# Optimization experiments

Measured on AMD Instinct MI355X. Metric: run time of the kernel, lower is better.

## Reference

```python
import jax, jax.numpy as jnp
import numpy as np

B = 2048
IN_FEATURES = 512
OUT_FEATURES = 32768
S = 64.0   # arcface default scale
M = 0.5    # arcface default margin
EPS = 1e-7


def _l2_normalize(x, axis=-1):
    # matches torch F.normalize(p=2, eps=1e-12)
    n = jnp.sqrt(jnp.sum(x * x, axis=axis, keepdims=True))
    return x / jnp.maximum(n, 1e-12)


def setup_inputs() -> dict:
    key = jax.random.key(0)
    k1, k2, k3 = jax.random.split(key, 3)
    features = jax.random.normal(k1, (B, IN_FEATURES), dtype=jnp.float32)
    y_true = jax.random.randint(k2, (B,), 0, OUT_FEATURES)
    # xavier_uniform_ for weight of shape (out, in)
    limit = float(np.sqrt(6.0 / (OUT_FEATURES + IN_FEATURES)))
    weight = jax.random.uniform(k3, (OUT_FEATURES, IN_FEATURES), dtype=jnp.float32,
                                minval=-limit, maxval=limit)
    return {"features": features, "y_true": y_true, "weight": weight}


def reference(features, y_true, weight):
    f = _l2_normalize(features)            # [B, D]
    w = _l2_normalize(weight)              # [C, D]
    wf = jnp.einsum('bd,cd->bc', f, w)     # [B, C] cosine logits
    tgt = wf[jnp.arange(wf.shape[0]), y_true]  # [B]
    # arcface margin transform
    numerator = S * jnp.cos(jnp.arccos(jnp.clip(tgt, -1.0 + EPS, 1.0 - EPS)) + M)
    # sum of exp(s*wf) over all non-target classes = full sum minus target term
    excl_sum = jnp.sum(jnp.exp(S * wf), axis=1) - jnp.exp(S * tgt)
    denominator = jnp.exp(numerator) + excl_sum
    L = numerator - jnp.log(denominator)
    return -jnp.mean(L)
```

## Files before the change

kernel.cpp:

```cpp
#include <hip/hip_runtime.h>
#include <hip/hip_bf16.h>
#include <math.h>


#define BN 2048
#define DK 512
#define CN 32768

typedef __attribute__((ext_vector_type(4))) float floatx4;
typedef __attribute__((ext_vector_type(2))) long longx2;

__device__ inline float dot4(floatx4 a, floatx4 b) {
  return a.x * b.x + a.y * b.y + a.z * b.z + a.w * b.w;
}

__device__ inline int pack_fp8x4(floatx4 v) {
  int r = __builtin_amdgcn_cvt_pk_fp8_f32(v.x, v.y, 0, false);
  r = __builtin_amdgcn_cvt_pk_fp8_f32(v.z, v.w, r, true);
  return r;
}

__device__ inline int permute16(int j) {
  return ((j >> 1) & 3) * 4 + (j >> 3) * 2 + (j & 1);
}

__device__ inline void async_ld16(const void* g, void* l) {
  __builtin_amdgcn_global_load_lds(
      (const __attribute__((address_space(1))) void*)g,
      (__attribute__((address_space(3))) void*)l, 16, 0, 0);
}

__global__ void prep_kernel(const float* __restrict__ feat,
                            const int* __restrict__ y,
                            const float* __restrict__ w,
                            int* __restrict__ fb8,
                            int* __restrict__ wb8,
                            float* __restrict__ tgt,
                            float* __restrict__ rowsum) {
  const int wave = threadIdx.x >> 6;
  const int l = threadIdx.x & 63;
  const int d0 = ((l >> 4) * 16)     + permute16(l & 15);
  const int d1 = ((4 + (l >> 4)) * 16) + permute16(l & 15);
  if (blockIdx.x < 8192) {
    const int row = blockIdx.x * 4 + wave;
    const floatx4* src = (const floatx4*)(w + (size_t)row * DK);
    floatx4 v0 = src[l];
    floatx4 v1 = src[64 + l];
    float s = dot4(v0, v0) + dot4(v1, v1);
#pragma unroll
    for (int off = 1; off < 64; off <<= 1) s += __shfl_xor(s, off, 64);
    const float scale = 1.0f / fmaxf(sqrtf(s), 1e-12f);
    v0 *= scale; v1 *= scale;
    int* db = wb8 + (size_t)row * 128;
    db[d0] = pack_fp8x4(v0);
    db[d1] = pack_fp8x4(v1);
  } else {
    const int i = (blockIdx.x - 8192) * 4 + wave;
    const floatx4* src = (const floatx4*)(feat + (size_t)i * DK);
    floatx4 v0 = src[l];
    floatx4 v1 = src[64 + l];
    const int cls = y[i];
    const floatx4* wr = (const floatx4*)(w + (size_t)cls * DK);
    floatx4 w0 = wr[l], w1 = wr[64 + l];
    float s  = dot4(v0, v0) + dot4(v1, v1);
    float d  = dot4(v0, w0) + dot4(v1, w1);
    float wn = dot4(w0, w0) + dot4(w1, w1);
#pragma unroll
    for (int off = 1; off < 64; off <<= 1) {
      s  += __shfl_xor(s, off, 64);
      d  += __shfl_xor(d, off, 64);
      wn += __shfl_xor(wn, off, 64);
    }
    const float fscale = 1.0f / fmaxf(sqrtf(s), 1e-12f);
    v0 *= fscale; v1 *= fscale;
    int* db = fb8 + (size_t)i * 128;
    db[d0] = pack_fp8x4(v0);
    db[d1] = pack_fp8x4(v1);
    if (l == 0) {
      tgt[i] = d * fscale / fmaxf(sqrtf(wn), 1e-12f);
      rowsum[i] = 0.0f;
    }
  }
}

__launch_bounds__(512, 4)
__global__ void gemm_exp_kernel(const char* __restrict__ fb8,
                                const char* __restrict__ wb8,
                                float* __restrict__ rowsum) {
  __shared__ char As[128 * 64];
  __shared__ char Bs[256 * 64];
  __shared__ float lsum[128];

  const int tid  = threadIdx.x;
  const int wave = tid >> 6;
  const int lane = tid & 63;

  const int n = blockIdx.x;
  const int tileM = ((n >> 3) & 15) * 128;
  const int tileN = (((n >> 7) << 3) | (n & 7)) * 256;

  const int wm = (wave >> 2) * 64;
  const int wn = (wave & 3) * 64;

  if (tid < 128) lsum[tid] = 0.0f;

  floatx4 acc[4][4];
#pragma unroll
  for (int mi = 0; mi < 4; ++mi)
#pragma unroll
    for (int ni = 0; ni < 4; ++ni)
      acc[mi][ni] = (floatx4){0.f, 0.f, 0.f, 0.f};

  const int mA = tid >> 2;
  const int uA = (tid & 3) ^ ((mA >> 1) & 3);
  const int mB0 = tid >> 2;
  const int uB0 = (tid & 3) ^ ((mB0 >> 1) & 3);
  const int mB1 = (512 + tid) >> 2;
  const int uB1 = (tid & 3) ^ ((mB1 >> 1) & 3);
  const char* gA  = fb8 + (size_t)(tileM + mA)  * DK + uA  * 16;
  const char* gB0 = wb8 + (size_t)(tileN + mB0) * DK + uB0 * 16;
  const char* gB1 = wb8 + (size_t)(tileN + mB1) * DK + uB1 * 16;
  char* lA  = &As[wave * 1024];
  char* lB0 = &Bs[wave * 1024];
  char* lB1 = &Bs[8192 + wave * 1024];

  const int mrow = lane & 15;
  const int q    = lane >> 4;

  for (int kk = 0; kk < DK / 64; ++kk) {
    __syncthreads();
    async_ld16(gA,  lA);
    async_ld16(gB0, lB0);
    async_ld16(gB1, lB1);
    gA += 64; gB0 += 64; gB1 += 64;
    __syncthreads();

    long af0[4], af1[4], bf0[4], bf1[4];
#pragma unroll
    for (int mi = 0; mi < 4; ++mi) {
      const int row = wm + mi * 16 + mrow;
      const int st = q ^ ((row >> 1) & 3);
      longx2 t = *(const longx2*)&As[row * 64 + st * 16];
      af0[mi] = t.x; af1[mi] = t.y;
    }
#pragma unroll
    for (int ni = 0; ni < 4; ++ni) {
      const int row = wn + ni * 16 + mrow;
      const int st = q ^ ((row >> 1) & 3);
      longx2 t = *(const longx2*)&Bs[row * 64 + st * 16];
      bf0[ni] = t.x; bf1[ni] = t.y;
    }
#pragma unroll
    for (int mi = 0; mi < 4; ++mi)
#pragma unroll
      for (int ni = 0; ni < 4; ++ni)
        acc[mi][ni] = __builtin_amdgcn_mfma_f32_16x16x32_fp8_fp8(
            af0[mi], bf0[ni], acc[mi][ni], 0, 0, 0);
#pragma unroll
    for (int mi = 0; mi < 4; ++mi)
#pragma unroll
      for (int ni = 0; ni < 4; ++ni)
        acc[mi][ni] = __builtin_amdgcn_mfma_f32_16x16x32_fp8_fp8(
            af1[mi], bf1[ni], acc[mi][ni], 0, 0, 0);
  }

  const int rowq = (lane >> 4) * 4;
#pragma unroll
  for (int mi = 0; mi < 4; ++mi) {
#pragma unroll
    for (int r = 0; r < 4; ++r) {
      float v = 0.f;
#pragma unroll
      for (int ni = 0; ni < 4; ++ni)
        v += __expf(64.0f * acc[mi][ni][r]);
      v += __shfl_xor(v, 1, 64);
      v += __shfl_xor(v, 2, 64);
      v += __shfl_xor(v, 4, 64);
      v += __shfl_xor(v, 8, 64);
      if ((lane & 15) == 0)
        atomicAdd(&lsum[wm + mi * 16 + rowq + r], v);
    }
  }
  __syncthreads();
  if (tid < 128)
    atomicAdd(&rowsum[tileM + tid], lsum[tid]);
}

__global__ void loss_kernel(const float* __restrict__ tgt,
                            const float* __restrict__ rowsum,
                            float* __restrict__ out) {
  __shared__ float wsum[8];
  const int t = threadIdx.x;
  float sum = 0.f;
  const float cM = 0.87758256189037271f;
  const float sM = 0.47942553860420301f;
  for (int i = t; i < BN; i += 512) {
    const float tg_raw = tgt[i];
    const float tg = fminf(fmaxf(tg_raw, -1.f + 1e-7f), 1.f - 1e-7f);
    const float num = 64.f * (tg * cM - sqrtf(fmaxf(1.f - tg * tg, 0.f)) * sM);
    const float den = expf(num) + rowsum[i] - expf(64.f * tg_raw);
    sum += num - logf(den);
  }
#pragma unroll
  for (int off = 1; off < 64; off <<= 1) sum += __shfl_xor(sum, off, 64);
  if ((t & 63) == 0) wsum[t >> 6] = sum;
  __syncthreads();
  if (t == 0) {
    float tot = 0.f;
#pragma unroll
    for (int k = 0; k < 8; ++k) tot += wsum[k];
    out[0] = -tot * (1.0f / (float)BN);
  }
}

extern "C" void kernel_launch(void* const* d_in, const int* in_sizes, int n_in,
                              void* d_out, int out_size, void* d_ws, size_t ws_size,
                              hipStream_t stream) {
  const float* features = (const float*)d_in[0];
  const int*   y_true   = (const int*)d_in[1];
  const float* weight   = (const float*)d_in[2];
  float* out = (float*)d_out;

  char* ws = (char*)d_ws;
  char* wb8    = ws;
  char* fb8    = ws + 16777216;
  float* tgt    = (float*)(ws + 17825792);
  float* rowsum = (float*)(ws + 17833984);

  prep_kernel<<<8192 + 512, 256, 0, stream>>>(features, y_true, weight,
                                              (int*)fb8, (int*)wb8, tgt, rowsum);
  gemm_exp_kernel<<<2048, 512, 0, stream>>>(fb8, wb8, rowsum);
  loss_kernel<<<1, 512, 0, stream>>>(tgt, rowsum, out);
}
```

Baseline: 158.6 us.

## Double-buffer LDS tiles in the FP8 GEMM to overlap async loads with MFMA

The GEMM kernel's shared tiles become two buffers. The next K-slice is prefetched with global_load_lds while MFMAs run on the current slice, which drops one barrier per iteration and hides global-load latency. The swizzled LDS read offsets are now computed once outside the loop and the K loop is fully unrolled. LDS use per block roughly doubles, which may lower the number of resident blocks per CU below what the launch bounds request.

```diff
diff --git a/kernel.cpp b/kernel.cpp
--- a/kernel.cpp
+++ b/kernel.cpp
@@ -39,7 +39,7 @@
                             float* __restrict__ rowsum) {
   const int wave = threadIdx.x >> 6;
   const int l = threadIdx.x & 63;
-  const int d0 = ((l >> 4) * 16)     + permute16(l & 15);
+  const int d0 = ((l >> 4) * 16)       + permute16(l & 15);
   const int d1 = ((4 + (l >> 4)) * 16) + permute16(l & 15);
   if (blockIdx.x < 8192) {
     const int row = blockIdx.x * 4 + wave;
@@ -87,8 +87,8 @@
 __global__ void gemm_exp_kernel(const char* __restrict__ fb8,
                                 const char* __restrict__ wb8,
                                 float* __restrict__ rowsum) {
-  __shared__ char As[128 * 64];
-  __shared__ char Bs[256 * 64];
+  __shared__ char As[2][128 * 64];
+  __shared__ char Bs[2][256 * 64];
   __shared__ float lsum[128];
 
   const int tid  = threadIdx.x;
@@ -113,41 +113,57 @@
 
   const int mA = tid >> 2;
   const int uA = (tid & 3) ^ ((mA >> 1) & 3);
-  const int mB0 = tid >> 2;
-  const int uB0 = (tid & 3) ^ ((mB0 >> 1) & 3);
   const int mB1 = (512 + tid) >> 2;
   const int uB1 = (tid & 3) ^ ((mB1 >> 1) & 3);
   const char* gA  = fb8 + (size_t)(tileM + mA)  * DK + uA  * 16;
-  const char* gB0 = wb8 + (size_t)(tileN + mB0) * DK + uB0 * 16;
+  const char* gB0 = wb8 + (size_t)(tileN + mA)  * DK + uA  * 16;
   const char* gB1 = wb8 + (size_t)(tileN + mB1) * DK + uB1 * 16;
-  char* lA  = &As[wave * 1024];
-  char* lB0 = &Bs[wave * 1024];
-  char* lB1 = &Bs[8192 + wave * 1024];
+  const int ldsA  = wave * 1024;
+  const int ldsB0 = wave * 1024;
+  const int ldsB1 = 8192 + wave * 1024;
 
   const int mrow = lane & 15;
   const int q    = lane >> 4;
-
+  int offA[4], offB[4];
+#pragma unroll
+  for (int mi = 0; mi < 4; ++mi) {
+    const int row = wm + mi * 16 + mrow;
+    offA[mi] = row * 64 + (q ^ ((row >> 1) & 3)) * 16;
+  }
+#pragma unroll
+  for (int ni = 0; ni < 4; ++ni) {
+    const int row = wn + ni * 16 + mrow;
+    offB[ni] = row * 64 + (q ^ ((row >> 1) & 3)) * 16;
+  }
+
+  async_ld16(gA,  &As[0][ldsA]);
+  async_ld16(gB0, &Bs[0][ldsB0]);
+  async_ld16(gB1, &Bs[0][ldsB1]);
+  gA += 64; gB0 += 64; gB1 += 64;
+
+#pragma unroll
   for (int kk = 0; kk < DK / 64; ++kk) {
+    const int cur = kk & 1;
     __syncthreads();
-    async_ld16(gA,  lA);
-    async_ld16(gB0, lB0);
-    async_ld16(gB1, lB1);
-    gA += 64; gB0 += 64; gB1 += 64;
-    __syncthreads();
-
+    if (kk < DK / 64 - 1) {
+      const int nxt = cur ^ 1;
+      async_ld16(gA,  &As[nxt][ldsA]);
+      async_ld16(gB0, &Bs[nxt][ldsB0]);
+      async_ld16(gB1, &Bs[nxt][ldsB1]);
+      gA += 64; gB0 += 64; gB1 += 64;
+    }
+
+    const char* Ab = As[cur];
+    const char* Bb = Bs[cur];
     long af0[4], af1[4], bf0[4], bf1[4];
 #pragma unroll
     for (int mi = 0; mi < 4; ++mi) {
-      const int row = wm + mi * 16 + mrow;
-      const int st = q ^ ((row >> 1) & 3);
-      longx2 t = *(const longx2*)&As[row * 64 + st * 16];
+      longx2 t = *(const longx2*)(Ab + offA[mi]);
       af0[mi] = t.x; af1[mi] = t.y;
     }
 #pragma unroll
     for (int ni = 0; ni < 4; ++ni) {
-      const int row = wn + ni * 16 + mrow;
-      const int st = q ^ ((row >> 1) & 3);
-      longx2 t = *(const longx2*)&Bs[row * 64 + st * 16];
+      longx2 t = *(const longx2*)(Bb + offB[ni]);
       bf0[ni] = t.x; bf1[ni] = t.y;
     }
 #pragma unroll
```

Result: faster. 154.9 us (-2.4%).
